# Kernel optimization log

Hardware: AMD Instinct MI355X
Metric: run time of the kernel (lower is better)

The kernel has to match this reference:

```python
import jax, jax.numpy as jnp
import numpy as np

ALPHA = 0.3      # keras LeakyReLU default
BN_EPS = 1e-3    # keras BatchNormalization default
RF, STRIDE = 8, 8


def leaky(x):
    return jnp.where(x >= 0, x, ALPHA * x)


def batchnorm(x, gamma, beta):
    # training-mode BN (train_flag=True): batch statistics over N,H,W
    mean = jnp.mean(x, axis=(0, 1, 2), keepdims=True)
    var = jnp.var(x, axis=(0, 1, 2), keepdims=True)
    return gamma * (x - mean) * jax.lax.rsqrt(var + BN_EPS) + beta


def cbl(x, W, gamma, beta):
    y = jax.lax.conv_general_dilated(x, W, (1, 1), 'SAME',
                                     dimension_numbers=('NHWC', 'HWIO', 'NHWC'))
    return leaky(batchnorm(y, gamma, beta))


def tcbl(x, W, gamma, beta):
    y = jax.lax.conv_transpose(x, W, (2, 2), 'SAME',
                               dimension_numbers=('NHWC', 'HWIO', 'NHWC'))
    return leaky(batchnorm(y, gamma, beta))


def setup_inputs() -> dict:
    key = jax.random.key(0)
    ks = jax.random.split(key, 8)
    B, H, W, C = 8, 128, 128, 128
    nH = (H - RF) // STRIDE + 1
    nW = (W - RF) // STRIDE + 1
    nWin = nH * nW  # 256
    inputs = jax.random.normal(ks[0], (B, H, W, C), dtype=jnp.float32)
    conv_scale = 1.0 / np.sqrt(3 * 3 * C)
    Wq = jax.random.normal(ks[1], (3, 3, C, 128), dtype=jnp.float32) * conv_scale
    Wk = jax.random.normal(ks[2], (3, 3, C, 128), dtype=jnp.float32) * conv_scale
    beta_bias = jax.random.normal(ks[3], (1, 1, 1, nWin), dtype=jnp.float32) * 0.05
    Wt = jax.random.normal(ks[4], (4, 4, nWin, 128), dtype=jnp.float32) / np.sqrt(4 * 4 * nWin)
    return {
        'inputs': inputs,
        'Wq': Wq, 'gq': jnp.ones((128,), jnp.float32), 'bq': jnp.zeros((128,), jnp.float32),
        'Wk': Wk, 'gk': jnp.ones((128,), jnp.float32), 'bk': jnp.zeros((128,), jnp.float32),
        'beta_bias': beta_bias,
        'g1': jnp.ones((nWin,), jnp.float32), 'b1': jnp.zeros((nWin,), jnp.float32),
        'Wt': Wt, 'gt': jnp.ones((128,), jnp.float32), 'bt': jnp.zeros((128,), jnp.float32),
    }


def reference(inputs, Wq, gq, bq, Wk, gk, bk, beta_bias, g1, b1, Wt, gt, bt):
    Q = cbl(inputs, Wq, gq, bq)   # (B,H,W,C)
    K = cbl(inputs, Wk, gk, bk)
    B, H, W, C = Q.shape
    nH = (H - RF) // STRIDE + 1
    nW = (W - RF) // STRIDE + 1
    # window start indices -> (n, RF) gather index grids
    hh = (jnp.arange(nH) * STRIDE)[:, None] + jnp.arange(RF)[None, :]
    ww = (jnp.arange(nW) * STRIDE)[:, None] + jnp.arange(RF)[None, :]

    def patches(x):
        # (B, nH, nW, RF, RF, C) -> (B, nWin, RF*RF*C)
        p = x[:, hh[:, None, :, None], ww[None, :, None, :], :]
        return p.reshape(B, nH * nW, RF * RF * C)

    Qp = patches(Q)
    Kp = patches(K)
    # sim[b, f, q] = <K window f, Q window q>; collapses the 4-nested loop
    sim = jnp.einsum('bfd,bqd->bfq', Kp, Qp).reshape(B, nH, nW, nH * nW)
    sim = sim + beta_bias
    act = leaky(batchnorm(sim, g1, b1))
    return tcbl(act, Wt, gt, bt)  # (B, 2*nH, 2*nW, 128)
```

## Files before the change

kernel.cpp:

```cpp
#include <hip/hip_runtime.h>

typedef __attribute__((ext_vector_type(8))) short bf16x8;
typedef __attribute__((ext_vector_type(8))) unsigned short u16x8;
typedef __attribute__((ext_vector_type(4))) float f32x4;

__device__ __forceinline__ unsigned short f2b(float x) {
    unsigned int u = __float_as_uint(x);
    u += 0x7FFFu + ((u >> 16) & 1u);
    return (unsigned short)(u >> 16);
}
__device__ __forceinline__ float b2f(unsigned short h) {
    return __uint_as_float(((unsigned int)h) << 16);
}
__device__ __forceinline__ float lrelu(float v) { return v >= 0.f ? v : 0.3f * v; }

#define GLL(gp, lp) __builtin_amdgcn_global_load_lds( \
    (const __attribute__((address_space(1))) unsigned int*)(gp), \
    (__attribute__((address_space(3))) unsigned int*)(lp), 16, 0, 0)


__global__ __launch_bounds__(256) void k0a_prep(
        const float* __restrict__ Wq, const float* __restrict__ Wk,
        const float* __restrict__ Wt, unsigned short* __restrict__ WqT,
        unsigned short* __restrict__ WkT, unsigned short* __restrict__ WtT,
        float* __restrict__ S) {
    int idx = blockIdx.x * 256 + threadIdx.x;
    int gs = gridDim.x * 256;
    for (int i = idx; i < 2048; i += gs) S[i] = 0.f;
    for (int i = idx; i < 147456; i += gs) {
        int tap = i >> 14, r = i & 16383, ci = r >> 7, co = r & 127;
        int ch = ci >> 6, e = ci & 63;
        int dst = ((tap * 2 + ch) * 128 + co) * 64 + (((e >> 3) ^ (co & 7)) << 3) + (e & 7);
        WqT[dst] = f2b(Wq[i]);
        WkT[dst] = f2b(Wk[i]);
    }
    for (int i = idx; i < 524288; i += gs) {
        int t = i >> 15, r = i & 32767, ci = r >> 7, co = r & 127;
        WtT[(((size_t)t << 7) + co) * 256 + ci] = f2b(Wt[i]);
    }
}

__global__ __launch_bounds__(256) void k0b_padx(const float* __restrict__ X,
                                                unsigned short* __restrict__ Xb) {
    int c = blockIdx.x * 256 + threadIdx.x;
    int k8 = c & 7;
    int t = c >> 3;
    int wp = t % 130; t /= 130;
    int ch = t & 1; t >>= 1;
    int hp = t % 130; int b = t / 130;
    u16x8 o;
    if (hp >= 1 && hp <= 128 && wp >= 1 && wp <= 128) {
        const float* s = X + (((size_t)(b * 128 + hp - 1) * 128) + (wp - 1)) * 128 + ch * 64 + k8 * 8;
        float4 f0 = *(const float4*)(s);
        float4 f1 = *(const float4*)(s + 4);
        o[0] = f2b(f0.x); o[1] = f2b(f0.y); o[2] = f2b(f0.z); o[3] = f2b(f0.w);
        o[4] = f2b(f1.x); o[5] = f2b(f1.y); o[6] = f2b(f1.z); o[7] = f2b(f1.w);
    } else {
#pragma unroll
        for (int j = 0; j < 8; ++j) o[j] = 0;
    }
    *(u16x8*)&Xb[(size_t)c * 8] = o;
}

__global__ __launch_bounds__(512, 4) void k1_conv(
        const unsigned short* __restrict__ Xb,
        const unsigned short* __restrict__ WqT, const unsigned short* __restrict__ WkT,
        unsigned short* __restrict__ Qraw, unsigned short* __restrict__ Kraw,
        float* __restrict__ S) {
    __shared__ unsigned short s_row[2 * 130 * 72];
    __shared__ unsigned short s_w[2][128 * 64];
    __shared__ float s_st[256];
    const int tid = threadIdx.x;
    const int x = blockIdx.x;
    const int conv = x & 1, hp = (x >> 1) & 63, b = x >> 7;
    const int h0 = hp * 2;
    const int lane = tid & 63, wv = tid >> 6;
    const int wm = wv & 3, wn = wv >> 2;
    const int l15 = lane & 15, kof = (lane >> 4) * 8;
    const int ar = wm >> 1;
    const int awb = (wm & 1) * 64;
    const int nb = wn * 64;

    const unsigned short* W = conv ? WkT : WqT;
    const int gofs = wv * 2048 + lane * 16;

    f32x4 acc[4][4];
#pragma unroll
    for (int i = 0; i < 4; ++i)
#pragma unroll
        for (int j = 0; j < 4; ++j) acc[i][j] = (f32x4){0.f, 0.f, 0.f, 0.f};
    if (tid < 256) s_st[tid] = 0.f;

    {
        const char* src = (const char*)W;
        char* dst = (char*)&s_w[0][0] + wv * 2048;
        GLL(src + gofs, dst);
        GLL(src + gofs + 1024, dst + 1024);
    }

#pragma unroll
    for (int ch = 0; ch < 2; ++ch) {
#pragma unroll
        for (int dy = 0; dy < 3; ++dy) {
#pragma unroll
            for (int dx = 0; dx < 3; ++dx) {
                const int p = (ch * 3 + dy) * 3 + dx;
                __builtin_amdgcn_s_barrier();
                if (dx == 0) {
                    const unsigned short* src0 = Xb + (size_t)((b * 130 + h0 + dy) * 2 + ch) * 8320;
                    const unsigned short* src1 = Xb + (size_t)((b * 130 + h0 + dy + 1) * 2 + ch) * 8320;
                    for (int c = tid; c < 2080; c += 512) {
                        int r = (c >= 1040);
                        int cw = r ? c - 1040 : c;
                        int w = cw >> 3, k8 = cw & 7;
                        *(u16x8*)&s_row[(r * 130 + w) * 72 + k8 * 8] =
                            *(const u16x8*)&((r ? src1 : src0)[cw * 8]);
                    }
                }
                if (p < 17) {
                    const int pn = p + 1;
                    const int nch = pn / 9, ntap = pn % 9;
                    const char* src = (const char*)(W + ((size_t)(ntap * 2 + nch) << 13));
                    char* dst = (char*)&s_w[pn & 1][0] + wv * 2048;
                    GLL(src + gofs, dst);
                    GLL(src + gofs + 1024, dst + 1024);
                    asm volatile("s_waitcnt vmcnt(2) lgkmcnt(0)" ::: "memory");
                } else {
                    asm volatile("s_waitcnt vmcnt(0) lgkmcnt(0)" ::: "memory");
                }
                __builtin_amdgcn_sched_barrier(0);
                __builtin_amdgcn_s_barrier();
                const unsigned short* wb = &s_w[p & 1][0];
#pragma unroll
                for (int kc = 0; kc < 2; ++kc) {
                    const int ci = kc * 32 + kof;
                    bf16x8 a[4], bb[4];
#pragma unroll
                    for (int mf = 0; mf < 4; ++mf)
                        a[mf] = *(const bf16x8*)&s_row[(ar * 130 + awb + mf * 16 + l15 + dx) * 72 + ci];
#pragma unroll
                    for (int nf = 0; nf < 4; ++nf) {
                        int co = nb + nf * 16 + l15;
                        bb[nf] = *(const bf16x8*)&wb[co * 64 + (((ci >> 3) ^ (co & 7)) << 3)];
                    }
#pragma unroll
                    for (int mf = 0; mf < 4; ++mf)
#pragma unroll
                        for (int nf = 0; nf < 4; ++nf)
                            acc[mf][nf] = __builtin_amdgcn_mfma_f32_16x16x32_bf16(
                                a[mf], bb[nf], acc[mf][nf], 0, 0, 0);
                }
            }
        }
    }
    __syncthreads();
    unsigned short* obase = conv ? Kraw : Qraw;
    const int h = h0 + ar;
    float sl[4] = {0.f, 0.f, 0.f, 0.f}, ssl[4] = {0.f, 0.f, 0.f, 0.f};
#pragma unroll
    for (int mf = 0; mf < 4; ++mf)
#pragma unroll
        for (int nf = 0; nf < 4; ++nf)
#pragma unroll
            for (int r = 0; r < 4; ++r) {
                float v = acc[mf][nf][r];
                int w = awb + mf * 16 + (lane >> 4) * 4 + r;
                int co = nb + nf * 16 + l15;
                obase[((size_t)(b * 128 + h) * 128 + w) * 128 + co] = f2b(v);
                sl[nf] += v; ssl[nf] += v * v;
            }
#pragma unroll
    for (int nf = 0; nf < 4; ++nf) {
        float s = sl[nf], ss = ssl[nf];
        s += __shfl_xor(s, 16); s += __shfl_xor(s, 32);
        ss += __shfl_xor(ss, 16); ss += __shfl_xor(ss, 32);
        if (lane < 16) {
            int chn = nb + nf * 16 + lane;
            atomicAdd(&s_st[chn], s);
            atomicAdd(&s_st[128 + chn], ss);
        }
    }
    __syncthreads();
    if (tid < 256) {
        int dst = (tid < 128) ? (conv * 128 + tid) : (256 + conv * 128 + (tid - 128));
        atomicAdd(&S[dst], s_st[tid]);
    }
}

__global__ void k2a_fin(const float* __restrict__ gq, const float* __restrict__ bq,
                        const float* __restrict__ gk, const float* __restrict__ bk,
                        const float* __restrict__ S, float* __restrict__ P) {
    int c = threadIdx.x;
    const float inv_n = 1.f / 131072.f;
    float mean = S[c] * inv_n;
    float var = S[256 + c] * inv_n - mean * mean;
    float g  = (c < 128) ? gq[c] : gk[c - 128];
    float be = (c < 128) ? bq[c] : bk[c - 128];
    float sc = g * rsqrtf(var + 1e-3f);
    P[c] = sc;
    P[256 + c] = be - mean * sc;
}

__global__ __launch_bounds__(512, 2) void k3_sim(const unsigned short* __restrict__ Qp,
                                                 const unsigned short* __restrict__ Kp,
                                                 const float* __restrict__ P,
                                                 float* __restrict__ part) {
    __shared__ unsigned short sA[128 * 136];
    __shared__ unsigned short sB[128 * 136];
    const int tid = threadIdx.x;
    const int x = blockIdx.x;
    const int kc = x & 15, ni = (x >> 4) & 1, mi = (x >> 5) & 1, b = x >> 6;
    const int lane = tid & 63, wv = tid >> 6;
    const int wm = wv & 1, wn = wv >> 1;
    f32x4 acc[4][2];
#pragma unroll
    for (int i = 0; i < 4; ++i)
#pragma unroll
        for (int j = 0; j < 2; ++j) acc[i][j] = (f32x4){0.f, 0.f, 0.f, 0.f};
    const int kof = (lane >> 4) * 8;
    const int arow = wm * 64 + (lane & 15);
    const int brow = wn * 32 + (lane & 15);

    for (int s = 0; s < 4; ++s) {
        const int p = kc * 4 + s, py = p >> 3, px = p & 7;
        __syncthreads();
        for (int c = tid; c < 2048; c += 512) {
            int r = c >> 4, k8 = c & 15;
            int cb = k8 * 8;
            int f = mi * 128 + r;
            size_t sa = ((size_t)(b * 128 + ((f >> 4) * 8 + py)) * 128 + ((f & 15) * 8 + px)) * 128 + cb;
            int q = ni * 128 + r;
            size_t sb = ((size_t)(b * 128 + ((q >> 4) * 8 + py)) * 128 + ((q & 15) * 8 + px)) * 128 + cb;
            u16x8 va = *(const u16x8*)&Kp[sa];
            u16x8 vb = *(const u16x8*)&Qp[sb];
            u16x8 oa, ob;
#pragma unroll
            for (int j = 0; j < 8; ++j) {
                float fk = b2f(va[j]);
                fk = lrelu(P[128 + cb + j] * fk + P[384 + cb + j]);
                oa[j] = f2b(fk);
                float fq = b2f(vb[j]);
                fq = lrelu(P[cb + j] * fq + P[256 + cb + j]);
                ob[j] = f2b(fq);
            }
            *(u16x8*)&sA[r * 136 + cb] = oa;
            *(u16x8*)&sB[r * 136 + cb] = ob;
        }
        __syncthreads();
#pragma unroll
        for (int k4 = 0; k4 < 4; ++k4) {
            const int ci = k4 * 32 + kof;
            bf16x8 a[4], bb[2];
#pragma unroll
            for (int mf = 0; mf < 4; ++mf)
                a[mf] = *(const bf16x8*)&sA[(arow + mf * 16) * 136 + ci];
#pragma unroll
            for (int nf = 0; nf < 2; ++nf)
                bb[nf] = *(const bf16x8*)&sB[(brow + nf * 16) * 136 + ci];
#pragma unroll
            for (int mf = 0; mf < 4; ++mf)
#pragma unroll
                for (int nf = 0; nf < 2; ++nf)
                    acc[mf][nf] = __builtin_amdgcn_mfma_f32_16x16x32_bf16(
                        a[mf], bb[nf], acc[mf][nf], 0, 0, 0);
        }
    }
    const size_t base = (size_t)(kc * 8 + b) * 65536;
#pragma unroll
    for (int mf = 0; mf < 4; ++mf)
#pragma unroll
        for (int nf = 0; nf < 2; ++nf)
#pragma unroll
            for (int r = 0; r < 4; ++r) {
                int f = mi * 128 + wm * 64 + mf * 16 + (lane >> 4) * 4 + r;
                int q = ni * 128 + wn * 32 + nf * 16 + (lane & 15);
                part[base + (size_t)f * 256 + q] = acc[mf][nf][r];
            }
}

__global__ __launch_bounds__(256) void k4_red(const float* __restrict__ part,
                                              const float* __restrict__ beta,
                                              float* __restrict__ sim, float* __restrict__ S) {
    int row0 = blockIdx.x * 8;
    int q = threadIdx.x;
    float bsum = 0.f, bss = 0.f;
    float bb = beta[q];
    for (int rr = 0; rr < 8; ++rr) {
        int row = row0 + rr;
        float s = 0.f;
#pragma unroll
        for (int kcc = 0; kcc < 16; ++kcc)
            s += part[(size_t)kcc * 524288 + (size_t)row * 256 + q];
        s += bb;
        sim[(size_t)row * 256 + q] = s;
        bsum += s; bss += s * s;
    }
    atomicAdd(&S[512 + q], bsum);
    atomicAdd(&S[768 + q], bss);
}

__global__ void k5a_fin(const float* __restrict__ g1, const float* __restrict__ b1,
                        const float* __restrict__ S, float* __restrict__ P) {
    int c = threadIdx.x;
    const float inv_n = 1.f / 2048.f;
    float mean = S[512 + c] * inv_n;
    float var = S[768 + c] * inv_n - mean * mean;
    float sc = g1[c] * rsqrtf(var + 1e-3f);
    P[512 + c] = sc;
    P[768 + c] = b1[c] - mean * sc;
}

__global__ __launch_bounds__(256) void k5b_act(const float* __restrict__ sim,
                                               const float* __restrict__ P,
                                               unsigned short* __restrict__ actp) {
    int c = blockIdx.x * 256 + threadIdx.x;
    int k8 = c & 31;
    int t = c >> 5;
    int jp = t % 18; t /= 18;
    int ip = t % 18; int b = t / 18;
    u16x8 o;
    if (ip >= 1 && ip <= 16 && jp >= 1 && jp <= 16) {
        int f = (ip - 1) * 16 + (jp - 1);
        const float* s = sim + (size_t)(b * 256 + f) * 256 + k8 * 8;
#pragma unroll
        for (int j = 0; j < 8; ++j) {
            int ci = k8 * 8 + j;
            o[j] = f2b(lrelu(P[512 + ci] * s[j] + P[768 + ci]));
        }
    } else {
#pragma unroll
        for (int j = 0; j < 8; ++j) o[j] = 0;
    }
    *(u16x8*)&actp[(size_t)c * 8] = o;
}

__global__ __launch_bounds__(512, 2) void k6_tconv(const unsigned short* __restrict__ actp,
                                                   const unsigned short* __restrict__ WtT,
                                                   float* __restrict__ y, float* __restrict__ S) {
    __shared__ unsigned short sA[64 * 264];
    __shared__ unsigned short sB[128 * 264];
    const int tid = threadIdx.x;
    const int x = blockIdx.x;
    const int iq = x & 3, pw = (x >> 2) & 1, ph = (x >> 3) & 1, b = x >> 4;
    const int lane = tid & 63, wv = tid >> 6;
    f32x4 acc[4];
#pragma unroll
    for (int i = 0; i < 4; ++i) acc[i] = (f32x4){0.f, 0.f, 0.f, 0.f};
    const int kof = (lane >> 4) * 8;
    const int arow = lane & 15;
    const int bco = wv * 16 + (lane & 15);

    for (int a2 = 0; a2 < 2; ++a2)
        for (int c2 = 0; c2 < 2; ++c2) {
            const int kh = ph + 2 * a2, kw = pw + 2 * c2;
            __syncthreads();
            for (int c = tid; c < 2048; c += 512) {
                int r = c >> 5, k8 = c & 31;
                int i = iq * 4 + (r >> 4), j = r & 15;
                size_t sa = (size_t)((b * 18 + (i + a2 + ph)) * 18 + (j + c2 + pw)) * 256 + k8 * 8;
                *(u16x8*)&sA[r * 264 + k8 * 8] = *(const u16x8*)&actp[sa];
            }
            for (int c = tid; c < 4096; c += 512) {
                int co = c >> 5, k8 = c & 31;
                size_t sb = (size_t)((kh * 4 + kw) * 128 + co) * 256 + k8 * 8;
                *(u16x8*)&sB[co * 264 + k8 * 8] = *(const u16x8*)&WtT[sb];
            }
            __syncthreads();
#pragma unroll
            for (int k8c = 0; k8c < 8; ++k8c) {
                const int ci = k8c * 32 + kof;
                bf16x8 bb = *(const bf16x8*)&sB[bco * 264 + ci];
#pragma unroll
                for (int mf = 0; mf < 4; ++mf) {
                    bf16x8 a = *(const bf16x8*)&sA[(arow + mf * 16) * 264 + ci];
                    acc[mf] = __builtin_amdgcn_mfma_f32_16x16x32_bf16(a, bb, acc[mf], 0, 0, 0);
                }
            }
        }
    float sl = 0.f, ssl = 0.f;
#pragma unroll
    for (int mf = 0; mf < 4; ++mf)
#pragma unroll
        for (int r = 0; r < 4; ++r) {
            float v = acc[mf][r];
            int m = mf * 16 + (lane >> 4) * 4 + r;
            int i = iq * 4 + (m >> 4), j = m & 15;
            int oh = 2 * i + ph, ow = 2 * j + pw;
            y[(size_t)((b * 32 + oh) * 32 + ow) * 128 + bco] = v;
            sl += v; ssl += v * v;
        }
    sl += __shfl_xor(sl, 16); sl += __shfl_xor(sl, 32);
    ssl += __shfl_xor(ssl, 16); ssl += __shfl_xor(ssl, 32);
    if (lane < 16) {
        atomicAdd(&S[1024 + wv * 16 + lane], sl);
        atomicAdd(&S[1152 + wv * 16 + lane], ssl);
    }
}

__global__ void k7_fin(const float* __restrict__ gt, const float* __restrict__ bt,
                       const float* __restrict__ S, float* __restrict__ P) {
    int c = threadIdx.x;
    const float inv_n = 1.f / 8192.f;
    float mean = S[1024 + c] * inv_n;
    float var = S[1152 + c] * inv_n - mean * mean;
    float sc = gt[c] * rsqrtf(var + 1e-3f);
    P[1024 + c] = sc;
    P[1280 + c] = bt[c] - mean * sc;
}

__global__ __launch_bounds__(256) void k8_out(const float* __restrict__ y,
                                              const float* __restrict__ P,
                                              float* __restrict__ out) {
    int c = blockIdx.x * 256 + threadIdx.x;
    const float4 v = *(const float4*)&y[(size_t)c * 4];
    int cb = (c & 31) * 4;
    float4 o;
    o.x = lrelu(P[1024 + cb + 0] * v.x + P[1280 + cb + 0]);
    o.y = lrelu(P[1024 + cb + 1] * v.y + P[1280 + cb + 1]);
    o.z = lrelu(P[1024 + cb + 2] * v.z + P[1280 + cb + 2]);
    o.w = lrelu(P[1024 + cb + 3] * v.w + P[1280 + cb + 3]);
    *(float4*)&out[(size_t)c * 4] = o;
}

extern "C" void kernel_launch(void* const* d_in, const int* in_sizes, int n_in,
                              void* d_out, int out_size, void* d_ws, size_t ws_size,
                              hipStream_t stream) {
    (void)in_sizes; (void)n_in; (void)out_size; (void)ws_size;
    const float* X    = (const float*)d_in[0];
    const float* Wq   = (const float*)d_in[1];
    const float* gq   = (const float*)d_in[2];
    const float* bq   = (const float*)d_in[3];
    const float* Wk   = (const float*)d_in[4];
    const float* gk   = (const float*)d_in[5];
    const float* bk   = (const float*)d_in[6];
    const float* beta = (const float*)d_in[7];
    const float* g1   = (const float*)d_in[8];
    const float* b1   = (const float*)d_in[9];
    const float* Wt   = (const float*)d_in[10];
    const float* gt   = (const float*)d_in[11];
    const float* bt   = (const float*)d_in[12];

    char* ws = (char*)d_ws;
    unsigned short* Qraw = (unsigned short*)(ws + 0ull);
    unsigned short* Kraw = (unsigned short*)(ws + 33554432ull);
    unsigned short* WqT  = (unsigned short*)(ws + 67108864ull);
    unsigned short* WkT  = (unsigned short*)(ws + 67403776ull);
    unsigned short* WtT  = (unsigned short*)(ws + 67698688ull);
    float* S             = (float*)(ws + 68747264ull);
    float* P             = (float*)(ws + 68755456ull);
    unsigned short* Xb   = (unsigned short*)(ws + 70858752ull);
    float* part          = (float*)(ws + 70858752ull);
    float* sim           = (float*)(ws + 0ull);
    unsigned short* actp = (unsigned short*)(ws + 4194304ull);
    float* y             = (float*)(ws + 8388608ull);
    float* out           = (float*)d_out;

    k0a_prep<<<1024, 256, 0, stream>>>(Wq, Wk, Wt, WqT, WkT, WtT, S);
    k0b_padx<<<8450, 256, 0, stream>>>(X, Xb);
    k1_conv<<<1024, 512, 0, stream>>>(Xb, WqT, WkT, Qraw, Kraw, S);
    k2a_fin<<<1, 256, 0, stream>>>(gq, bq, gk, bk, S, P);
    k3_sim<<<512, 512, 0, stream>>>(Qraw, Kraw, P, part);
    k4_red<<<256, 256, 0, stream>>>(part, beta, sim, S);
    k5a_fin<<<1, 256, 0, stream>>>(g1, b1, S, P);
    k5b_act<<<729, 256, 0, stream>>>(sim, P, actp);
    k6_tconv<<<128, 512, 0, stream>>>(actp, WtT, y, S);
    k7_fin<<<1, 128, 0, stream>>>(gt, bt, S, P);
    k8_out<<<1024, 256, 0, stream>>>(y, P, out);
}
```

Before: 178.5 us.

## Fold BN finalize kernels into consumers, remap blocks to XCDs, halve sim split-K

The three single-block BN finalize kernels are removed. Each consumer (k3_sim, k5b_act, k8_out) now recomputes scale and shift from the raw statistics into shared memory, which saves launches and serialization gaps. k1_conv and k3_sim block indices are remapped so that neighbouring work lands on the same XCD for better L2 locality. The sim split-K drops from 16 to 8 chunks (256 blocks, each doing 8 patch positions), which halves the partial-sum traffic that k4_red reduces but cuts parallelism. Every block also redundantly recomputes the BN parameters, which adds a little extra work per block.

New measurement: 170.4 us. 1.05x faster.

```diff
diff --git a/kernel.cpp b/kernel.cpp
--- a/kernel.cpp
+++ b/kernel.cpp
@@ -72,7 +72,9 @@
     __shared__ float s_st[256];
     const int tid = threadIdx.x;
     const int x = blockIdx.x;
-    const int conv = x & 1, hp = (x >> 1) & 63, b = x >> 7;
+    const int xcd = x & 7, sdec = x >> 3;
+    const int b = sdec >> 4, r16 = sdec & 15;
+    const int hp = xcd * 8 + (r16 >> 1), conv = r16 & 1;
     const int h0 = hp * 2;
     const int lane = tid & 63, wv = tid >> 6;
     const int wm = wv & 3, wn = wv >> 2;
@@ -187,31 +189,32 @@
     }
 }
 
-__global__ void k2a_fin(const float* __restrict__ gq, const float* __restrict__ bq,
-                        const float* __restrict__ gk, const float* __restrict__ bk,
-                        const float* __restrict__ S, float* __restrict__ P) {
-    int c = threadIdx.x;
-    const float inv_n = 1.f / 131072.f;
-    float mean = S[c] * inv_n;
-    float var = S[256 + c] * inv_n - mean * mean;
-    float g  = (c < 128) ? gq[c] : gk[c - 128];
-    float be = (c < 128) ? bq[c] : bk[c - 128];
-    float sc = g * rsqrtf(var + 1e-3f);
-    P[c] = sc;
-    P[256 + c] = be - mean * sc;
-}
-
 __global__ __launch_bounds__(512, 2) void k3_sim(const unsigned short* __restrict__ Qp,
                                                  const unsigned short* __restrict__ Kp,
-                                                 const float* __restrict__ P,
+                                                 const float* __restrict__ S,
+                                                 const float* __restrict__ gq, const float* __restrict__ bq,
+                                                 const float* __restrict__ gk, const float* __restrict__ bk,
                                                  float* __restrict__ part) {
     __shared__ unsigned short sA[128 * 136];
     __shared__ unsigned short sB[128 * 136];
+    __shared__ float s_p[512];
     const int tid = threadIdx.x;
     const int x = blockIdx.x;
-    const int kc = x & 15, ni = (x >> 4) & 1, mi = (x >> 5) & 1, b = x >> 6;
+    const int kc = x & 7, sdec = x >> 3;
+    const int b = sdec >> 2, mn = sdec & 3;
+    const int mi = mn >> 1, ni = mn & 1;
     const int lane = tid & 63, wv = tid >> 6;
     const int wm = wv & 1, wn = wv >> 1;
+    if (tid < 256) {
+        const float inv_n = 1.f / 131072.f;
+        float mean = S[tid] * inv_n;
+        float var = S[256 + tid] * inv_n - mean * mean;
+        float g  = (tid < 128) ? gq[tid] : gk[tid - 128];
+        float be = (tid < 128) ? bq[tid] : bk[tid - 128];
+        float sc = g * rsqrtf(var + 1e-3f);
+        s_p[tid] = sc;
+        s_p[256 + tid] = be - mean * sc;
+    }
     f32x4 acc[4][2];
 #pragma unroll
     for (int i = 0; i < 4; ++i)
@@ -221,8 +224,8 @@
     const int arow = wm * 64 + (lane & 15);
     const int brow = wn * 32 + (lane & 15);
 
-    for (int s = 0; s < 4; ++s) {
-        const int p = kc * 4 + s, py = p >> 3, px = p & 7;
+    for (int s = 0; s < 8; ++s) {
+        const int py = kc, px = s;
         __syncthreads();
         for (int c = tid; c < 2048; c += 512) {
             int r = c >> 4, k8 = c & 15;
@@ -237,10 +240,10 @@
 #pragma unroll
             for (int j = 0; j < 8; ++j) {
                 float fk = b2f(va[j]);
-                fk = lrelu(P[128 + cb + j] * fk + P[384 + cb + j]);
+                fk = lrelu(s_p[128 + cb + j] * fk + s_p[384 + cb + j]);
                 oa[j] = f2b(fk);
                 float fq = b2f(vb[j]);
-                fq = lrelu(P[cb + j] * fq + P[256 + cb + j]);
+                fq = lrelu(s_p[cb + j] * fq + s_p[256 + cb + j]);
                 ob[j] = f2b(fq);
             }
             *(u16x8*)&sA[r * 136 + cb] = oa;
@@ -289,7 +292,7 @@
         int row = row0 + rr;
         float s = 0.f;
 #pragma unroll
-        for (int kcc = 0; kcc < 16; ++kcc)
+        for (int kcc = 0; kcc < 8; ++kcc)
             s += part[(size_t)kcc * 524288 + (size_t)row * 256 + q];
         s += bb;
         sim[(size_t)row * 256 + q] = s;
@@ -299,21 +302,23 @@
     atomicAdd(&S[768 + q], bss);
 }
 
-__global__ void k5a_fin(const float* __restrict__ g1, const float* __restrict__ b1,
-                        const float* __restrict__ S, float* __restrict__ P) {
-    int c = threadIdx.x;
-    const float inv_n = 1.f / 2048.f;
-    float mean = S[512 + c] * inv_n;
-    float var = S[768 + c] * inv_n - mean * mean;
-    float sc = g1[c] * rsqrtf(var + 1e-3f);
-    P[512 + c] = sc;
-    P[768 + c] = b1[c] - mean * sc;
-}
-
 __global__ __launch_bounds__(256) void k5b_act(const float* __restrict__ sim,
-                                               const float* __restrict__ P,
+                                               const float* __restrict__ S,
+                                               const float* __restrict__ g1, const float* __restrict__ b1,
                                                unsigned short* __restrict__ actp) {
+    __shared__ float s_p[512];
+    {
+        int c = threadIdx.x;
+        const float inv_n = 1.f / 2048.f;
+        float mean = S[512 + c] * inv_n;
+        float var = S[768 + c] * inv_n - mean * mean;
+        float sc = g1[c] * rsqrtf(var + 1e-3f);
+        s_p[c] = sc;
+        s_p[256 + c] = b1[c] - mean * sc;
+    }
+    __syncthreads();
     int c = blockIdx.x * 256 + threadIdx.x;
+    if (c >= 186624) return;
     int k8 = c & 31;
     int t = c >> 5;
     int jp = t % 18; t /= 18;
@@ -325,7 +330,7 @@
 #pragma unroll
         for (int j = 0; j < 8; ++j) {
             int ci = k8 * 8 + j;
-            o[j] = f2b(lrelu(P[512 + ci] * s[j] + P[768 + ci]));
+            o[j] = f2b(lrelu(s_p[ci] * s[j] + s_p[256 + ci]));
         }
     } else {
 #pragma unroll
@@ -397,28 +402,29 @@
     }
 }
 
-__global__ void k7_fin(const float* __restrict__ gt, const float* __restrict__ bt,
-                       const float* __restrict__ S, float* __restrict__ P) {
-    int c = threadIdx.x;
-    const float inv_n = 1.f / 8192.f;
-    float mean = S[1024 + c] * inv_n;
-    float var = S[1152 + c] * inv_n - mean * mean;
-    float sc = gt[c] * rsqrtf(var + 1e-3f);
-    P[1024 + c] = sc;
-    P[1280 + c] = bt[c] - mean * sc;
-}
-
 __global__ __launch_bounds__(256) void k8_out(const float* __restrict__ y,
-                                              const float* __restrict__ P,
+                                              const float* __restrict__ S,
+                                              const float* __restrict__ gt, const float* __restrict__ bt,
                                               float* __restrict__ out) {
+    __shared__ float s_p[256];
+    if (threadIdx.x < 128) {
+        int c = threadIdx.x;
+        const float inv_n = 1.f / 8192.f;
+        float mean = S[1024 + c] * inv_n;
+        float var = S[1152 + c] * inv_n - mean * mean;
+        float sc = gt[c] * rsqrtf(var + 1e-3f);
+        s_p[c] = sc;
+        s_p[128 + c] = bt[c] - mean * sc;
+    }
+    __syncthreads();
     int c = blockIdx.x * 256 + threadIdx.x;
     const float4 v = *(const float4*)&y[(size_t)c * 4];
     int cb = (c & 31) * 4;
     float4 o;
-    o.x = lrelu(P[1024 + cb + 0] * v.x + P[1280 + cb + 0]);
-    o.y = lrelu(P[1024 + cb + 1] * v.y + P[1280 + cb + 1]);
-    o.z = lrelu(P[1024 + cb + 2] * v.z + P[1280 + cb + 2]);
-    o.w = lrelu(P[1024 + cb + 3] * v.w + P[1280 + cb + 3]);
+    o.x = lrelu(s_p[cb + 0] * v.x + s_p[128 + cb + 0]);
+    o.y = lrelu(s_p[cb + 1] * v.y + s_p[128 + cb + 1]);
+    o.z = lrelu(s_p[cb + 2] * v.z + s_p[128 + cb + 2]);
+    o.w = lrelu(s_p[cb + 3] * v.w + s_p[128 + cb + 3]);
     *(float4*)&out[(size_t)c * 4] = o;
 }
 
@@ -447,9 +453,8 @@
     unsigned short* WkT  = (unsigned short*)(ws + 67403776ull);
     unsigned short* WtT  = (unsigned short*)(ws + 67698688ull);
     float* S             = (float*)(ws + 68747264ull);
-    float* P             = (float*)(ws + 68755456ull);
-    unsigned short* Xb   = (unsigned short*)(ws + 70858752ull);
-    float* part          = (float*)(ws + 70858752ull);
+    unsigned short* Xb   = (unsigned short*)(ws + 68761600ull);
+    float* part          = (float*)(ws + 68761600ull);
     float* sim           = (float*)(ws + 0ull);
     unsigned short* actp = (unsigned short*)(ws + 4194304ull);
     float* y             = (float*)(ws + 8388608ull);
@@ -458,12 +463,9 @@
     k0a_prep<<<1024, 256, 0, stream>>>(Wq, Wk, Wt, WqT, WkT, WtT, S);
     k0b_padx<<<8450, 256, 0, stream>>>(X, Xb);
     k1_conv<<<1024, 512, 0, stream>>>(Xb, WqT, WkT, Qraw, Kraw, S);
-    k2a_fin<<<1, 256, 0, stream>>>(gq, bq, gk, bk, S, P);
-    k3_sim<<<512, 512, 0, stream>>>(Qraw, Kraw, P, part);
+    k3_sim<<<256, 512, 0, stream>>>(Qraw, Kraw, S, gq, bq, gk, bk, part);
     k4_red<<<256, 256, 0, stream>>>(part, beta, sim, S);
-    k5a_fin<<<1, 256, 0, stream>>>(g1, b1, S, P);
-    k5b_act<<<729, 256, 0, stream>>>(sim, P, actp);
+    k5b_act<<<729, 256, 0, stream>>>(sim, S, g1, b1, actp);
     k6_tconv<<<128, 512, 0, stream>>>(actp, WtT, y, S);
-    k7_fin<<<1, 128, 0, stream>>>(gt, bt, S, P);
-    k8_out<<<1024, 256, 0, stream>>>(y, P, out);
-}
+    k8_out<<<1024, 256, 0, stream>>>(y, S, gt, bt, out);
+}
```
